# Kernel optimization log

Measured on AMD Instinct MI355X. Metric: run time of the kernel, lower is better.

Reference implementation:

```python
import jax, jax.numpy as jnp
import numpy as np

# Faithful JAX reference for VoxelModule.forward.
# The torch module builds, per batch element, a dict mapping
#   key = vx*10000 + vy*100 + vz  (vx,vy,vz = int(coord * (voxel_size-1)))
# to the list of point indices falling in that voxel.
# Dicts are not jit-able; the equivalent parallel/sort-based grouping is:
#   keys        [B,N] : per-point voxel key (same integer math as torch)
#   order       [B,N] : stable argsort of keys -> point indices grouped by voxel
#   sorted_keys [B,N] : keys in grouped order (run boundaries delimit voxels)
# This (keys, order, sorted_keys) triple encodes exactly the same grouping
# information as the list-of-dicts output.

B = 16
N = 500_000
VOXEL_SIZE = 40  # keys require per-axis index < 100, so voxel_size <= 100


def setup_inputs() -> dict:
    key = jax.random.key(0)
    point_cloud = jax.random.uniform(key, (B, N, 3), dtype=jnp.float32)  # coords in [0,1)
    return {"point_cloud": point_cloud, "voxel_size": VOXEL_SIZE}


def reference(point_cloud, voxel_size):
    # int(x) in Python truncates toward zero; coords are non-negative so
    # truncation == floor. astype(int32) truncates, matching torch code.
    idx = (point_cloud * (voxel_size - 1)).astype(jnp.int32)  # [B,N,3]
    keys = idx[..., 0] * 10000 + idx[..., 1] * 100 + idx[..., 2]  # [B,N]
    # Stable sort: within a voxel, point indices stay in ascending order,
    # matching the append order of the torch dict-building loop.
    order = jnp.argsort(keys, axis=-1, stable=True)  # [B,N] grouped point ids
    sorted_keys = jnp.take_along_axis(keys, order, axis=-1)  # [B,N]
    return keys, order, sorted_keys
```

## Files before the change

### kernel.cpp

```cpp
#include <hip/hip_runtime.h>


#define B 16
#define N 500000
#define BN (B * N)
#define NC2 122
#define RELB 512
#define CAP2 4736
#define TPB1 512
#define NW1 (TPB1 / 64)
#define PPB 8192
#define NG 4
#define CPB ((N + PPB - 1) / PPB)
#define NIT4 3

__global__ __launch_bounds__(TPB1) void pass1(const float* __restrict__ pc,
                                              const int* __restrict__ vs,
                                              int* __restrict__ keys,
                                              int* __restrict__ ccnt,
                                              int* __restrict__ staged) {
    int b = blockIdx.x / CPB;
    int chunk = blockIdx.x % CPB;
    int t = threadIdx.x;
    int w = t >> 6;
    int lane = t & 63;
    __shared__ int lh[NW1][NC2];
    __shared__ int lst[NC2];
    __shared__ int gadj[NC2];
    __shared__ int lim[NC2];
    __shared__ int buf[PPB];
    for (int k = lane; k < NC2; k += 64) lh[w][k] = 0;
    float scale = (float)(vs[0] - 1);
    long gb0 = (long)b * N;
    int pe[4 * NG];
#pragma unroll
    for (int g = 0; g < NG; ++g) {
        int i0 = chunk * PPB + g * 2048 + t * 4;
        if (i0 >= N) continue;
        const float4* F = (const float4*)(pc + 3 * (gb0 + i0));
        float4 f0 = F[0], f1 = F[1], f2 = F[2];
        float xs[4] = {f0.x, f0.w, f1.z, f2.y};
        float ys[4] = {f0.y, f1.x, f1.w, f2.z};
        float zs[4] = {f0.z, f1.y, f2.x, f2.w};
        int kk[4];
#pragma unroll
        for (int j = 0; j < 4; ++j) {
            int vx = (int)(xs[j] * scale);
            int vy = (int)(ys[j] * scale);
            int vz = (int)(zs[j] * scale);
            kk[j] = vx * 10000 + vy * 100 + vz;
            int lin = (vx * 40 + vy) * 40 + vz;
            int c2 = lin >> 9;
            int rv = atomicAdd(&lh[w][c2], 1);
            pe[4 * g + j] = ((lin & 511) << 20) | (c2 << 13) | rv;
        }
        int4 kv; kv.x = kk[0]; kv.y = kk[1]; kv.z = kk[2]; kv.w = kk[3];
        *(int4*)(keys + gb0 + i0) = kv;
    }
    __syncthreads();
    if (t < 64) {
        int idx0 = 2 * t, idx1 = 2 * t + 1;
        int run0 = 0, run1 = 0;
        if (idx0 < NC2) {
#pragma unroll
            for (int ww = 0; ww < NW1; ++ww) { int v = lh[ww][idx0]; lh[ww][idx0] = run0; run0 += v; }
#pragma unroll
            for (int ww = 0; ww < NW1; ++ww) { int v = lh[ww][idx1]; lh[ww][idx1] = run1; run1 += v; }
        }
        int s = run0 + run1;
        int x = s;
#pragma unroll
        for (int d = 1; d < 64; d <<= 1) { int y = __shfl_up(x, d, 64); if (t >= d) x += y; }
        int excl = x - s;
        if (idx0 < NC2) {
            int l0 = excl, l1 = excl + run0;
            lst[idx0] = l0; lst[idx1] = l1;
            int g0 = run0 ? atomicAdd(&ccnt[b * NC2 + idx0], run0) : 0;
            int g1 = run1 ? atomicAdd(&ccnt[b * NC2 + idx1], run1) : 0;
            gadj[idx0] = idx0 * CAP2 + g0 - l0;
            gadj[idx1] = idx1 * CAP2 + g1 - l1;
            lim[idx0] = l0 + CAP2 - g0;
            lim[idx1] = l1 + CAP2 - g1;
        }
    }
    __syncthreads();
#pragma unroll
    for (int g = 0; g < NG; ++g) {
        int i0 = chunk * PPB + g * 2048 + t * 4;
        if (i0 >= N) continue;
#pragma unroll
        for (int j = 0; j < 4; ++j) {
            int e = pe[4 * g + j];
            int c2 = (e >> 13) & 127;
            int rv = e & 8191;
            int rel = e >> 20;
            int pos = lst[c2] + lh[w][c2] + rv;
            buf[pos] = (c2 << 22) | (rel << 13) | (g * 2048 + t * 4 + j);
        }
    }
    __syncthreads();
    int nval = N - chunk * PPB; if (nval > PPB) nval = PPB;
    int ibase = chunk * PPB;
    long sbase = (long)b * NC2 * CAP2;
#pragma unroll
    for (int q = 0; q < PPB / TPB1; ++q) {
        int p = t + q * TPB1;
        if (p < nval) {
            int e = buf[p];
            int c = e >> 22;
            int rel = (e >> 13) & 511;
            int local = e & 8191;
            if (p < lim[c]) staged[sbase + gadj[c] + p] = (rel << 19) | (ibase + local);
        }
    }
}

__global__ __launch_bounds__(512) void pass2(const int* __restrict__ ccnt,
                                             const int* __restrict__ staged,
                                             int* __restrict__ order_out,
                                             int* __restrict__ skeys_out) {
    int bc = blockIdx.x;
    int b = bc / NC2;
    int c2 = bc % NC2;
    int t = threadIdx.x;
    __shared__ int h[RELB];
    __shared__ int st[RELB + 1];
    __shared__ int skeyL[RELB];
    __shared__ int srt[CAP2];
    __shared__ int bsh;
    int cnt = ccnt[bc]; if (cnt > CAP2) cnt = CAP2;
    if (cnt == 0) return;

    {
        int z = t;
        h[z] = 0;
        int lin = (c2 << 9) + z;
        int vx = lin / 1600;
        int r = lin - vx * 1600;
        int vy = r / 40;
        int vz = r - vy * 40;
        skeyL[z] = vx * 10000 + vy * 100 + vz;
    }
    if (t < 64) {
        int idx0 = 2 * t, idx1 = 2 * t + 1;
        int v0 = 0, v1 = 0;
        if (idx0 < NC2) {
            v0 = ccnt[b * NC2 + idx0]; if (v0 > CAP2) v0 = CAP2;
            v1 = ccnt[b * NC2 + idx1]; if (v1 > CAP2) v1 = CAP2;
        }
        int s = v0 + v1;
        int x = s;
#pragma unroll
        for (int d = 1; d < 64; d <<= 1) { int y = __shfl_up(x, d, 64); if (t >= d) x += y; }
        int excl = x - s;
        if (idx0 == c2) bsh = excl;
        if (idx1 == c2) bsh = excl + v0;
    }
    __syncthreads();

    long rb = (long)bc * CAP2;
    const int4* reg4 = (const int4*)(staged + rb);
    int n4 = cnt >> 2;
    int4 ev4[NIT4];
#pragma unroll
    for (int q = 0; q < NIT4; ++q) {
        int p4 = t + q * 512;
        if (p4 < n4) {
            int4 e = reg4[p4];
            ev4[q] = e;
            atomicAdd(&h[e.x >> 19], 1);
            atomicAdd(&h[e.y >> 19], 1);
            atomicAdd(&h[e.z >> 19], 1);
            atomicAdd(&h[e.w >> 19], 1);
        }
    }
    int evt = 0; bool tv = false;
    {
        int p = (n4 << 2) + t;
        if (p < cnt) { evt = staged[rb + p]; tv = true; atomicAdd(&h[evt >> 19], 1); }
    }
    __syncthreads();

    if (t < 64) {
        int vals[8]; int s = 0;
#pragma unroll
        for (int j = 0; j < 8; ++j) { int v = h[8 * t + j]; vals[j] = s; s += v; }
        int x = s;
#pragma unroll
        for (int d = 1; d < 64; d <<= 1) { int y = __shfl_up(x, d, 64); if (t >= d) x += y; }
        int excl = x - s;
#pragma unroll
        for (int j = 0; j < 8; ++j) { st[8 * t + j] = excl + vals[j]; h[8 * t + j] = 0; }
        if (t == 63) st[RELB] = x;
    }
    __syncthreads();

#pragma unroll
    for (int q = 0; q < NIT4; ++q) {
        int p4 = t + q * 512;
        if (p4 < n4) {
            int4 e = ev4[q];
            int z0 = e.x >> 19; srt[st[z0] + atomicAdd(&h[z0], 1)] = e.x;
            int z1 = e.y >> 19; srt[st[z1] + atomicAdd(&h[z1], 1)] = e.y;
            int z2 = e.z >> 19; srt[st[z2] + atomicAdd(&h[z2], 1)] = e.z;
            int z3 = e.w >> 19; srt[st[z3] + atomicAdd(&h[z3], 1)] = e.w;
        }
    }
    if (tv) { int z = evt >> 19; srt[st[z] + atomicAdd(&h[z], 1)] = evt; }
    __syncthreads();

    long ob = (long)b * N + bsh;
    for (int p = t; p < cnt; p += 512) {
        int v = srt[p];
        int z = v >> 19;
        int s = st[z], e2 = st[z + 1];
        int rank = 0;
        for (int j = s; j < e2; ++j) rank += (srt[j] < v);
        order_out[ob + s + rank] = v & 0x7FFFF;
        skeys_out[ob + s + rank] = skeyL[z];
    }
}

extern "C" void kernel_launch(void* const* d_in, const int* in_sizes, int n_in,
                              void* d_out, int out_size, void* d_ws, size_t ws_size,
                              hipStream_t stream) {
    const float* pc = (const float*)d_in[0];
    const int* vs = (const int*)d_in[1];
    int* out = (int*)d_out;
    int* keys_out = out;
    int* order_out = out + BN;
    int* skeys_out = out + 2 * BN;

    int* ccnt = (int*)d_ws;
    int* staged = ccnt + B * NC2;

    (void)hipMemsetAsync(ccnt, 0, (size_t)B * NC2 * sizeof(int), stream);
    pass1<<<B * CPB, TPB1, 0, stream>>>(pc, vs, keys_out, ccnt, staged);
    pass2<<<B * NC2, 512, 0, stream>>>(ccnt, staged, order_out, skeys_out);
}
```

Baseline: 214.0 us.

## Fuse both passes into one kernel with per-batch spin barrier

Merges the binning pass and the per-bucket sort pass into a single persistent-style kernel. Blocks of each batch signal completion through an atomic counter and spin until all chunks of that batch finish, then each block sorts up to two coarse buckets, reusing one shared memory region. This removes a kernel launch and the grid-wide gap between passes, and lets batches progress independently. It relies on all blocks of a batch being co-resident, so it risks deadlock or stalls if occupancy is too low, and busy-waiting blocks hold compute units.

```diff
diff --git a/kernel.cpp b/kernel.cpp
--- a/kernel.cpp
+++ b/kernel.cpp
@@ -13,211 +13,226 @@
 #define NG 4
 #define CPB ((N + PPB - 1) / PPB)
 #define NIT4 3
-
-__global__ __launch_bounds__(TPB1) void pass1(const float* __restrict__ pc,
-                                              const int* __restrict__ vs,
-                                              int* __restrict__ keys,
-                                              int* __restrict__ ccnt,
-                                              int* __restrict__ staged) {
-    int b = blockIdx.x / CPB;
-    int chunk = blockIdx.x % CPB;
+#define SMEM_WORDS (NW1 * NC2 + 3 * NC2 + PPB)
+
+__global__ __launch_bounds__(TPB1, 8) void fused(
+    const float* __restrict__ pc, const int* __restrict__ vs,
+    int* __restrict__ keys, int* __restrict__ ccnt, int* __restrict__ done,
+    int* __restrict__ staged, int* __restrict__ order_out,
+    int* __restrict__ skeys_out) {
+    int blk = blockIdx.x;
+    int b = blk / CPB;
+    int chunk = blk % CPB;
     int t = threadIdx.x;
     int w = t >> 6;
     int lane = t & 63;
-    __shared__ int lh[NW1][NC2];
-    __shared__ int lst[NC2];
-    __shared__ int gadj[NC2];
-    __shared__ int lim[NC2];
-    __shared__ int buf[PPB];
-    for (int k = lane; k < NC2; k += 64) lh[w][k] = 0;
-    float scale = (float)(vs[0] - 1);
-    long gb0 = (long)b * N;
-    int pe[4 * NG];
-#pragma unroll
-    for (int g = 0; g < NG; ++g) {
-        int i0 = chunk * PPB + g * 2048 + t * 4;
-        if (i0 >= N) continue;
-        const float4* F = (const float4*)(pc + 3 * (gb0 + i0));
-        float4 f0 = F[0], f1 = F[1], f2 = F[2];
-        float xs[4] = {f0.x, f0.w, f1.z, f2.y};
-        float ys[4] = {f0.y, f1.x, f1.w, f2.z};
-        float zs[4] = {f0.z, f1.y, f2.x, f2.w};
-        int kk[4];
-#pragma unroll
-        for (int j = 0; j < 4; ++j) {
-            int vx = (int)(xs[j] * scale);
-            int vy = (int)(ys[j] * scale);
-            int vz = (int)(zs[j] * scale);
-            kk[j] = vx * 10000 + vy * 100 + vz;
-            int lin = (vx * 40 + vy) * 40 + vz;
-            int c2 = lin >> 9;
-            int rv = atomicAdd(&lh[w][c2], 1);
-            pe[4 * g + j] = ((lin & 511) << 20) | (c2 << 13) | rv;
-        }
-        int4 kv; kv.x = kk[0]; kv.y = kk[1]; kv.z = kk[2]; kv.w = kk[3];
-        *(int4*)(keys + gb0 + i0) = kv;
+    __shared__ int smem[SMEM_WORDS];
+    __shared__ int bsh;
+
+    {
+        int (*lh)[NC2] = (int(*)[NC2])smem;
+        int* lst = smem + NW1 * NC2;
+        int* gadj = lst + NC2;
+        int* lim = gadj + NC2;
+        int* buf = lim + NC2;
+        for (int k = lane; k < NC2; k += 64) lh[w][k] = 0;
+        float scale = (float)(vs[0] - 1);
+        long gb0 = (long)b * N;
+        int pe[4 * NG];
+#pragma unroll
+        for (int g = 0; g < NG; ++g) {
+            int i0 = chunk * PPB + g * 2048 + t * 4;
+            if (i0 >= N) continue;
+            const float4* F = (const float4*)(pc + 3 * (gb0 + i0));
+            float4 f0 = F[0], f1 = F[1], f2 = F[2];
+            float xs[4] = {f0.x, f0.w, f1.z, f2.y};
+            float ys[4] = {f0.y, f1.x, f1.w, f2.z};
+            float zs[4] = {f0.z, f1.y, f2.x, f2.w};
+            int kk[4];
+#pragma unroll
+            for (int j = 0; j < 4; ++j) {
+                int vx = (int)(xs[j] * scale);
+                int vy = (int)(ys[j] * scale);
+                int vz = (int)(zs[j] * scale);
+                kk[j] = vx * 10000 + vy * 100 + vz;
+                int lin = (vx * 40 + vy) * 40 + vz;
+                int c2 = lin >> 9;
+                int rv = atomicAdd(&lh[w][c2], 1);
+                pe[4 * g + j] = ((lin & 511) << 20) | (c2 << 13) | rv;
+            }
+            int4 kv; kv.x = kk[0]; kv.y = kk[1]; kv.z = kk[2]; kv.w = kk[3];
+            *(int4*)(keys + gb0 + i0) = kv;
+        }
+        __syncthreads();
+        if (t < 64) {
+            int idx0 = 2 * t, idx1 = 2 * t + 1;
+            int run0 = 0, run1 = 0;
+            if (idx0 < NC2) {
+#pragma unroll
+                for (int ww = 0; ww < NW1; ++ww) { int v = lh[ww][idx0]; lh[ww][idx0] = run0; run0 += v; }
+#pragma unroll
+                for (int ww = 0; ww < NW1; ++ww) { int v = lh[ww][idx1]; lh[ww][idx1] = run1; run1 += v; }
+            }
+            int s = run0 + run1;
+            int x = s;
+#pragma unroll
+            for (int d = 1; d < 64; d <<= 1) { int y = __shfl_up(x, d, 64); if (t >= d) x += y; }
+            int excl = x - s;
+            if (idx0 < NC2) {
+                int l0 = excl, l1 = excl + run0;
+                lst[idx0] = l0; lst[idx1] = l1;
+                int g0 = run0 ? atomicAdd(&ccnt[b * NC2 + idx0], run0) : 0;
+                int g1 = run1 ? atomicAdd(&ccnt[b * NC2 + idx1], run1) : 0;
+                gadj[idx0] = idx0 * CAP2 + g0 - l0;
+                gadj[idx1] = idx1 * CAP2 + g1 - l1;
+                lim[idx0] = l0 + CAP2 - g0;
+                lim[idx1] = l1 + CAP2 - g1;
+            }
+        }
+        __syncthreads();
+#pragma unroll
+        for (int g = 0; g < NG; ++g) {
+            int i0 = chunk * PPB + g * 2048 + t * 4;
+            if (i0 >= N) continue;
+#pragma unroll
+            for (int j = 0; j < 4; ++j) {
+                int e = pe[4 * g + j];
+                int c2 = (e >> 13) & 127;
+                int rv = e & 8191;
+                int rel = e >> 20;
+                int pos = lst[c2] + lh[w][c2] + rv;
+                buf[pos] = (c2 << 22) | (rel << 13) | (g * 2048 + t * 4 + j);
+            }
+        }
+        __syncthreads();
+        int nval = N - chunk * PPB; if (nval > PPB) nval = PPB;
+        int ibase = chunk * PPB;
+        long sbase = (long)b * NC2 * CAP2;
+#pragma unroll
+        for (int q = 0; q < PPB / TPB1; ++q) {
+            int p = t + q * TPB1;
+            if (p < nval) {
+                int e = buf[p];
+                int c = e >> 22;
+                int rel = (e >> 13) & 511;
+                int local = e & 8191;
+                if (p < lim[c]) staged[sbase + gadj[c] + p] = (rel << 19) | (ibase + local);
+            }
+        }
     }
     __syncthreads();
-    if (t < 64) {
-        int idx0 = 2 * t, idx1 = 2 * t + 1;
-        int run0 = 0, run1 = 0;
-        if (idx0 < NC2) {
-#pragma unroll
-            for (int ww = 0; ww < NW1; ++ww) { int v = lh[ww][idx0]; lh[ww][idx0] = run0; run0 += v; }
-#pragma unroll
-            for (int ww = 0; ww < NW1; ++ww) { int v = lh[ww][idx1]; lh[ww][idx1] = run1; run1 += v; }
-        }
-        int s = run0 + run1;
-        int x = s;
-#pragma unroll
-        for (int d = 1; d < 64; d <<= 1) { int y = __shfl_up(x, d, 64); if (t >= d) x += y; }
-        int excl = x - s;
-        if (idx0 < NC2) {
-            int l0 = excl, l1 = excl + run0;
-            lst[idx0] = l0; lst[idx1] = l1;
-            int g0 = run0 ? atomicAdd(&ccnt[b * NC2 + idx0], run0) : 0;
-            int g1 = run1 ? atomicAdd(&ccnt[b * NC2 + idx1], run1) : 0;
-            gadj[idx0] = idx0 * CAP2 + g0 - l0;
-            gadj[idx1] = idx1 * CAP2 + g1 - l1;
-            lim[idx0] = l0 + CAP2 - g0;
-            lim[idx1] = l1 + CAP2 - g1;
-        }
+    if (t == 0) {
+        __threadfence();
+        __hip_atomic_fetch_add(&done[b], 1, __ATOMIC_RELEASE, __HIP_MEMORY_SCOPE_AGENT);
+        while (__hip_atomic_load(&done[b], __ATOMIC_RELAXED, __HIP_MEMORY_SCOPE_AGENT) < CPB)
+            __builtin_amdgcn_s_sleep(2);
+        __threadfence();
     }
     __syncthreads();
-#pragma unroll
-    for (int g = 0; g < NG; ++g) {
-        int i0 = chunk * PPB + g * 2048 + t * 4;
-        if (i0 >= N) continue;
-#pragma unroll
-        for (int j = 0; j < 4; ++j) {
-            int e = pe[4 * g + j];
-            int c2 = (e >> 13) & 127;
-            int rv = e & 8191;
-            int rel = e >> 20;
-            int pos = lst[c2] + lh[w][c2] + rv;
-            buf[pos] = (c2 << 22) | (rel << 13) | (g * 2048 + t * 4 + j);
-        }
-    }
-    __syncthreads();
-    int nval = N - chunk * PPB; if (nval > PPB) nval = PPB;
-    int ibase = chunk * PPB;
-    long sbase = (long)b * NC2 * CAP2;
-#pragma unroll
-    for (int q = 0; q < PPB / TPB1; ++q) {
-        int p = t + q * TPB1;
-        if (p < nval) {
-            int e = buf[p];
-            int c = e >> 22;
-            int rel = (e >> 13) & 511;
-            int local = e & 8191;
-            if (p < lim[c]) staged[sbase + gadj[c] + p] = (rel << 19) | (ibase + local);
-        }
-    }
-}
-
-__global__ __launch_bounds__(512) void pass2(const int* __restrict__ ccnt,
-                                             const int* __restrict__ staged,
-                                             int* __restrict__ order_out,
-                                             int* __restrict__ skeys_out) {
-    int bc = blockIdx.x;
-    int b = bc / NC2;
-    int c2 = bc % NC2;
-    int t = threadIdx.x;
-    __shared__ int h[RELB];
-    __shared__ int st[RELB + 1];
-    __shared__ int skeyL[RELB];
-    __shared__ int srt[CAP2];
-    __shared__ int bsh;
-    int cnt = ccnt[bc]; if (cnt > CAP2) cnt = CAP2;
-    if (cnt == 0) return;
 
     {
-        int z = t;
-        h[z] = 0;
-        int lin = (c2 << 9) + z;
-        int vx = lin / 1600;
-        int r = lin - vx * 1600;
-        int vy = r / 40;
-        int vz = r - vy * 40;
-        skeyL[z] = vx * 10000 + vy * 100 + vz;
-    }
-    if (t < 64) {
-        int idx0 = 2 * t, idx1 = 2 * t + 1;
-        int v0 = 0, v1 = 0;
-        if (idx0 < NC2) {
-            v0 = ccnt[b * NC2 + idx0]; if (v0 > CAP2) v0 = CAP2;
-            v1 = ccnt[b * NC2 + idx1]; if (v1 > CAP2) v1 = CAP2;
-        }
-        int s = v0 + v1;
-        int x = s;
-#pragma unroll
-        for (int d = 1; d < 64; d <<= 1) { int y = __shfl_up(x, d, 64); if (t >= d) x += y; }
-        int excl = x - s;
-        if (idx0 == c2) bsh = excl;
-        if (idx1 == c2) bsh = excl + v0;
-    }
-    __syncthreads();
-
-    long rb = (long)bc * CAP2;
-    const int4* reg4 = (const int4*)(staged + rb);
-    int n4 = cnt >> 2;
-    int4 ev4[NIT4];
-#pragma unroll
-    for (int q = 0; q < NIT4; ++q) {
-        int p4 = t + q * 512;
-        if (p4 < n4) {
-            int4 e = reg4[p4];
-            ev4[q] = e;
-            atomicAdd(&h[e.x >> 19], 1);
-            atomicAdd(&h[e.y >> 19], 1);
-            atomicAdd(&h[e.z >> 19], 1);
-            atomicAdd(&h[e.w >> 19], 1);
-        }
-    }
-    int evt = 0; bool tv = false;
-    {
-        int p = (n4 << 2) + t;
-        if (p < cnt) { evt = staged[rb + p]; tv = true; atomicAdd(&h[evt >> 19], 1); }
-    }
-    __syncthreads();
-
-    if (t < 64) {
-        int vals[8]; int s = 0;
-#pragma unroll
-        for (int j = 0; j < 8; ++j) { int v = h[8 * t + j]; vals[j] = s; s += v; }
-        int x = s;
-#pragma unroll
-        for (int d = 1; d < 64; d <<= 1) { int y = __shfl_up(x, d, 64); if (t >= d) x += y; }
-        int excl = x - s;
-#pragma unroll
-        for (int j = 0; j < 8; ++j) { st[8 * t + j] = excl + vals[j]; h[8 * t + j] = 0; }
-        if (t == 63) st[RELB] = x;
-    }
-    __syncthreads();
-
-#pragma unroll
-    for (int q = 0; q < NIT4; ++q) {
-        int p4 = t + q * 512;
-        if (p4 < n4) {
-            int4 e = ev4[q];
-            int z0 = e.x >> 19; srt[st[z0] + atomicAdd(&h[z0], 1)] = e.x;
-            int z1 = e.y >> 19; srt[st[z1] + atomicAdd(&h[z1], 1)] = e.y;
-            int z2 = e.z >> 19; srt[st[z2] + atomicAdd(&h[z2], 1)] = e.z;
-            int z3 = e.w >> 19; srt[st[z3] + atomicAdd(&h[z3], 1)] = e.w;
-        }
-    }
-    if (tv) { int z = evt >> 19; srt[st[z] + atomicAdd(&h[z], 1)] = evt; }
-    __syncthreads();
-
-    long ob = (long)b * N + bsh;
-    for (int p = t; p < cnt; p += 512) {
-        int v = srt[p];
-        int z = v >> 19;
-        int s = st[z], e2 = st[z + 1];
-        int rank = 0;
-        for (int j = s; j < e2; ++j) rank += (srt[j] < v);
-        order_out[ob + s + rank] = v & 0x7FFFF;
-        skeys_out[ob + s + rank] = skeyL[z];
+        int* h = smem;
+        int* st = smem + RELB;
+        int* skeyL = st + RELB + 1;
+        int* srt = skeyL + RELB;
+#pragma unroll 1
+        for (int it = 0; it < 2; ++it) {
+            int c2 = chunk + it * CPB;
+            if (c2 >= NC2) break;
+            int bc = b * NC2 + c2;
+            int cnt = ccnt[bc]; if (cnt > CAP2) cnt = CAP2;
+            __syncthreads();
+            if (cnt == 0) continue;
+
+            {
+                int z = t;
+                h[z] = 0;
+                int lin = (c2 << 9) + z;
+                int vx = lin / 1600;
+                int r = lin - vx * 1600;
+                int vy = r / 40;
+                int vz = r - vy * 40;
+                skeyL[z] = vx * 10000 + vy * 100 + vz;
+            }
+            if (t < 64) {
+                int idx0 = 2 * t, idx1 = 2 * t + 1;
+                int v0 = 0, v1 = 0;
+                if (idx0 < NC2) {
+                    v0 = ccnt[b * NC2 + idx0]; if (v0 > CAP2) v0 = CAP2;
+                    v1 = ccnt[b * NC2 + idx1]; if (v1 > CAP2) v1 = CAP2;
+                }
+                int s = v0 + v1;
+                int x = s;
+#pragma unroll
+                for (int d = 1; d < 64; d <<= 1) { int y = __shfl_up(x, d, 64); if (t >= d) x += y; }
+                int excl = x - s;
+                if (idx0 == c2) bsh = excl;
+                if (idx1 == c2) bsh = excl + v0;
+            }
+            __syncthreads();
+
+            long rb = (long)bc * CAP2;
+            const int4* reg4 = (const int4*)(staged + rb);
+            int n4 = cnt >> 2;
+            int4 ev4[NIT4];
+#pragma unroll
+            for (int q = 0; q < NIT4; ++q) {
+                int p4 = t + q * TPB1;
+                if (p4 < n4) {
+                    int4 e = reg4[p4];
+                    ev4[q] = e;
+                    atomicAdd(&h[e.x >> 19], 1);
+                    atomicAdd(&h[e.y >> 19], 1);
+                    atomicAdd(&h[e.z >> 19], 1);
+                    atomicAdd(&h[e.w >> 19], 1);
+                }
+            }
+            int evt = 0; bool tv = false;
+            {
+                int p = (n4 << 2) + t;
+                if (p < cnt) { evt = staged[rb + p]; tv = true; atomicAdd(&h[evt >> 19], 1); }
+            }
+            __syncthreads();
+
+            if (t < 64) {
+                int vals[8]; int s = 0;
+#pragma unroll
+                for (int j = 0; j < 8; ++j) { int v = h[8 * t + j]; vals[j] = s; s += v; }
+                int x = s;
+#pragma unroll
+                for (int d = 1; d < 64; d <<= 1) { int y = __shfl_up(x, d, 64); if (t >= d) x += y; }
+                int excl = x - s;
+#pragma unroll
+                for (int j = 0; j < 8; ++j) { st[8 * t + j] = excl + vals[j]; h[8 * t + j] = 0; }
+                if (t == 63) st[RELB] = x;
+            }
+            __syncthreads();
+
+#pragma unroll
+            for (int q = 0; q < NIT4; ++q) {
+                int p4 = t + q * TPB1;
+                if (p4 < n4) {
+                    int4 e = ev4[q];
+                    int z0 = e.x >> 19; srt[st[z0] + atomicAdd(&h[z0], 1)] = e.x;
+                    int z1 = e.y >> 19; srt[st[z1] + atomicAdd(&h[z1], 1)] = e.y;
+                    int z2 = e.z >> 19; srt[st[z2] + atomicAdd(&h[z2], 1)] = e.z;
+                    int z3 = e.w >> 19; srt[st[z3] + atomicAdd(&h[z3], 1)] = e.w;
+                }
+            }
+            if (tv) { int z = evt >> 19; srt[st[z] + atomicAdd(&h[z], 1)] = evt; }
+            __syncthreads();
+
+            long ob = (long)b * N + bsh;
+            for (int p = t; p < cnt; p += TPB1) {
+                int v = srt[p];
+                int z = v >> 19;
+                int s = st[z], e2 = st[z + 1];
+                int rank = 0;
+                for (int j = s; j < e2; ++j) rank += (srt[j] < v);
+                order_out[ob + s + rank] = v & 0x7FFFF;
+                skeys_out[ob + s + rank] = skeyL[z];
+            }
+        }
     }
 }
 
@@ -232,9 +247,10 @@
     int* skeys_out = out + 2 * BN;
 
     int* ccnt = (int*)d_ws;
-    int* staged = ccnt + B * NC2;
-
-    (void)hipMemsetAsync(ccnt, 0, (size_t)B * NC2 * sizeof(int), stream);
-    pass1<<<B * CPB, TPB1, 0, stream>>>(pc, vs, keys_out, ccnt, staged);
-    pass2<<<B * NC2, 512, 0, stream>>>(ccnt, staged, order_out, skeys_out);
+    int* done = ccnt + B * NC2;
+    int* staged = done + B;
+
+    (void)hipMemsetAsync(ccnt, 0, (size_t)(B * NC2 + B) * sizeof(int), stream);
+    fused<<<B * CPB, TPB1, 0, stream>>>(pc, vs, keys_out, ccnt, done, staged,
+                                        order_out, skeys_out);
 }
```

New measurement: 382.8 us. 1.79x slower.

## Replace global atomic bucket staging with per-chunk tables and contiguous chunk dumps

Applied to the files above, without the earlier changes.

Pass1 no longer claims global bucket slots with atomics. Each block writes its locally bucket-sorted chunk to staging as contiguous int4 stores and records a per-chunk table of bucket start offsets. Pass2 reads every chunk's offsets for its bucket, prefix-sums them, and gathers elements with a binary search over chunks. This drops the memset, the global atomics and the scattered staging writes. In exchange pass2 does scalar gathers with a per-element binary search, and the chunk index is now packed into fewer bits.

```diff
diff --git a/kernel.cpp b/kernel.cpp
--- a/kernel.cpp
+++ b/kernel.cpp
@@ -7,27 +7,26 @@
 #define NC2 122
 #define RELB 512
 #define CAP2 4736
-#define TPB1 512
-#define NW1 (TPB1 / 64)
+#define TPB 512
+#define NW1 (TPB / 64)
 #define PPB 8192
 #define NG 4
-#define CPB ((N + PPB - 1) / PPB)
-#define NIT4 3
-
-__global__ __launch_bounds__(TPB1) void pass1(const float* __restrict__ pc,
-                                              const int* __restrict__ vs,
-                                              int* __restrict__ keys,
-                                              int* __restrict__ ccnt,
-                                              int* __restrict__ staged) {
+#define CPB 62
+#define LSTROW 128
+#define NIT2 10
+
+__global__ __launch_bounds__(TPB, 8) void pass1(const float* __restrict__ pc,
+                                                const int* __restrict__ vs,
+                                                int* __restrict__ keys,
+                                                int* __restrict__ lstT,
+                                                int* __restrict__ staged) {
     int b = blockIdx.x / CPB;
     int chunk = blockIdx.x % CPB;
     int t = threadIdx.x;
     int w = t >> 6;
     int lane = t & 63;
     __shared__ int lh[NW1][NC2];
-    __shared__ int lst[NC2];
-    __shared__ int gadj[NC2];
-    __shared__ int lim[NC2];
+    __shared__ int lst[NC2 + 1];
     __shared__ int buf[PPB];
     for (int k = lane; k < NC2; k += 64) lh[w][k] = 0;
     float scale = (float)(vs[0] - 1);
@@ -52,7 +51,7 @@
             int lin = (vx * 40 + vy) * 40 + vz;
             int c2 = lin >> 9;
             int rv = atomicAdd(&lh[w][c2], 1);
-            pe[4 * g + j] = ((lin & 511) << 20) | (c2 << 13) | rv;
+            pe[4 * g + j] = (c2 << 22) | ((lin & 511) << 13) | rv;
         }
         int4 kv; kv.x = kk[0]; kv.y = kk[1]; kv.z = kk[2]; kv.w = kk[3];
         *(int4*)(keys + gb0 + i0) = kv;
@@ -72,16 +71,8 @@
 #pragma unroll
         for (int d = 1; d < 64; d <<= 1) { int y = __shfl_up(x, d, 64); if (t >= d) x += y; }
         int excl = x - s;
-        if (idx0 < NC2) {
-            int l0 = excl, l1 = excl + run0;
-            lst[idx0] = l0; lst[idx1] = l1;
-            int g0 = run0 ? atomicAdd(&ccnt[b * NC2 + idx0], run0) : 0;
-            int g1 = run1 ? atomicAdd(&ccnt[b * NC2 + idx1], run1) : 0;
-            gadj[idx0] = idx0 * CAP2 + g0 - l0;
-            gadj[idx1] = idx1 * CAP2 + g1 - l1;
-            lim[idx0] = l0 + CAP2 - g0;
-            lim[idx1] = l1 + CAP2 - g1;
-        }
+        if (idx0 < NC2) { lst[idx0] = excl; lst[idx1] = excl + run0; }
+        if (t == 63) lst[NC2] = x;
     }
     __syncthreads();
 #pragma unroll
@@ -91,31 +82,23 @@
 #pragma unroll
         for (int j = 0; j < 4; ++j) {
             int e = pe[4 * g + j];
-            int c2 = (e >> 13) & 127;
+            int c2 = e >> 22;
             int rv = e & 8191;
-            int rel = e >> 20;
+            int rel = (e >> 13) & 511;
             int pos = lst[c2] + lh[w][c2] + rv;
-            buf[pos] = (c2 << 22) | (rel << 13) | (g * 2048 + t * 4 + j);
-        }
-    }
-    __syncthreads();
-    int nval = N - chunk * PPB; if (nval > PPB) nval = PPB;
-    int ibase = chunk * PPB;
-    long sbase = (long)b * NC2 * CAP2;
-#pragma unroll
-    for (int q = 0; q < PPB / TPB1; ++q) {
-        int p = t + q * TPB1;
-        if (p < nval) {
-            int e = buf[p];
-            int c = e >> 22;
-            int rel = (e >> 13) & 511;
-            int local = e & 8191;
-            if (p < lim[c]) staged[sbase + gadj[c] + p] = (rel << 19) | (ibase + local);
-        }
-    }
+            buf[pos] = (rel << 13) | (g * 2048 + t * 4 + j);
+        }
+    }
+    if (t < NC2 + 1) lstT[(b * CPB + chunk) * LSTROW + t] = lst[t];
+    __syncthreads();
+    long sb4 = (long)(b * CPB + chunk) * (PPB / 4);
+    const int4* B4 = (const int4*)buf;
+    int4* S4 = (int4*)staged;
+#pragma unroll
+    for (int q = 0; q < PPB / TPB / 4; ++q) S4[sb4 + t + q * TPB] = B4[t + q * TPB];
 }
 
-__global__ __launch_bounds__(512) void pass2(const int* __restrict__ ccnt,
+__global__ __launch_bounds__(TPB) void pass2(const int* __restrict__ lstT,
                                              const int* __restrict__ staged,
                                              int* __restrict__ order_out,
                                              int* __restrict__ skeys_out) {
@@ -127,9 +110,9 @@
     __shared__ int st[RELB + 1];
     __shared__ int skeyL[RELB];
     __shared__ int srt[CAP2];
-    __shared__ int bsh;
-    int cnt = ccnt[bc]; if (cnt > CAP2) cnt = CAP2;
-    if (cnt == 0) return;
+    __shared__ int ofs[CPB + 1];
+    __shared__ int adj[CPB];
+    __shared__ int bshS, cntS;
 
     {
         int z = t;
@@ -142,53 +125,52 @@
         skeyL[z] = vx * 10000 + vy * 100 + vz;
     }
     if (t < 64) {
-        int idx0 = 2 * t, idx1 = 2 * t + 1;
-        int v0 = 0, v1 = 0;
-        if (idx0 < NC2) {
-            v0 = ccnt[b * NC2 + idx0]; if (v0 > CAP2) v0 = CAP2;
-            v1 = ccnt[b * NC2 + idx1]; if (v1 > CAP2) v1 = CAP2;
-        }
-        int s = v0 + v1;
+        int s0 = 0, s1 = 0;
+        if (t < CPB) {
+            const int* row = lstT + (b * CPB + t) * LSTROW;
+            s0 = row[c2]; s1 = row[c2 + 1];
+        }
+        int rl = s1 - s0;
+        int bs = s0;
+#pragma unroll
+        for (int d = 1; d < 64; d <<= 1) bs += __shfl_xor(bs, d, 64);
+        int x = rl;
+#pragma unroll
+        for (int d = 1; d < 64; d <<= 1) { int y = __shfl_up(x, d, 64); if (t >= d) x += y; }
+        int excl = x - rl;
+        if (t < CPB) { ofs[t] = excl; adj[t] = t * PPB + s0 - excl; }
+        if (t == CPB - 1) { ofs[CPB] = x; cntS = x; }
+        if (t == 0) bshS = bs;
+    }
+    __syncthreads();
+    int cnt = cntS; if (cnt > CAP2) cnt = CAP2;
+    if (cnt == 0) return;
+    int bsh = bshS;
+    long bbase = (long)b * (CPB * PPB);
+
+    int ev[NIT2];
+#pragma unroll
+    for (int q = 0; q < NIT2; ++q) {
+        int p = t + q * TPB;
+        if (p < cnt) {
+            int lo = 0, hi = CPB;
+            while (hi - lo > 1) { int mid = (lo + hi) >> 1; if (ofs[mid] <= p) lo = mid; else hi = mid; }
+            int e = staged[bbase + adj[lo] + p];
+            int v = ((e >> 13) << 19) | (lo << 13) | (e & 8191);
+            ev[q] = v;
+            atomicAdd(&h[v >> 19], 1);
+        }
+    }
+    __syncthreads();
+
+    if (t < 64) {
+        int vals[8]; int s = 0;
+#pragma unroll
+        for (int j = 0; j < 8; ++j) { int v = h[8 * t + j]; vals[j] = s; s += v; }
         int x = s;
 #pragma unroll
         for (int d = 1; d < 64; d <<= 1) { int y = __shfl_up(x, d, 64); if (t >= d) x += y; }
         int excl = x - s;
-        if (idx0 == c2) bsh = excl;
-        if (idx1 == c2) bsh = excl + v0;
-    }
-    __syncthreads();
-
-    long rb = (long)bc * CAP2;
-    const int4* reg4 = (const int4*)(staged + rb);
-    int n4 = cnt >> 2;
-    int4 ev4[NIT4];
-#pragma unroll
-    for (int q = 0; q < NIT4; ++q) {
-        int p4 = t + q * 512;
-        if (p4 < n4) {
-            int4 e = reg4[p4];
-            ev4[q] = e;
-            atomicAdd(&h[e.x >> 19], 1);
-            atomicAdd(&h[e.y >> 19], 1);
-            atomicAdd(&h[e.z >> 19], 1);
-            atomicAdd(&h[e.w >> 19], 1);
-        }
-    }
-    int evt = 0; bool tv = false;
-    {
-        int p = (n4 << 2) + t;
-        if (p < cnt) { evt = staged[rb + p]; tv = true; atomicAdd(&h[evt >> 19], 1); }
-    }
-    __syncthreads();
-
-    if (t < 64) {
-        int vals[8]; int s = 0;
-#pragma unroll
-        for (int j = 0; j < 8; ++j) { int v = h[8 * t + j]; vals[j] = s; s += v; }
-        int x = s;
-#pragma unroll
-        for (int d = 1; d < 64; d <<= 1) { int y = __shfl_up(x, d, 64); if (t >= d) x += y; }
-        int excl = x - s;
 #pragma unroll
         for (int j = 0; j < 8; ++j) { st[8 * t + j] = excl + vals[j]; h[8 * t + j] = 0; }
         if (t == 63) st[RELB] = x;
@@ -196,21 +178,19 @@
     __syncthreads();
 
 #pragma unroll
-    for (int q = 0; q < NIT4; ++q) {
-        int p4 = t + q * 512;
-        if (p4 < n4) {
-            int4 e = ev4[q];
-            int z0 = e.x >> 19; srt[st[z0] + atomicAdd(&h[z0], 1)] = e.x;
-            int z1 = e.y >> 19; srt[st[z1] + atomicAdd(&h[z1], 1)] = e.y;
-            int z2 = e.z >> 19; srt[st[z2] + atomicAdd(&h[z2], 1)] = e.z;
-            int z3 = e.w >> 19; srt[st[z3] + atomicAdd(&h[z3], 1)] = e.w;
-        }
-    }
-    if (tv) { int z = evt >> 19; srt[st[z] + atomicAdd(&h[z], 1)] = evt; }
+    for (int q = 0; q < NIT2; ++q) {
+        int p = t + q * TPB;
+        if (p < cnt) {
+            int v = ev[q];
+            int z = v >> 19;
+            int r = atomicAdd(&h[z], 1);
+            srt[st[z] + r] = v;
+        }
+    }
     __syncthreads();
 
     long ob = (long)b * N + bsh;
-    for (int p = t; p < cnt; p += 512) {
+    for (int p = t; p < cnt; p += TPB) {
         int v = srt[p];
         int z = v >> 19;
         int s = st[z], e2 = st[z + 1];
@@ -231,10 +211,9 @@
     int* order_out = out + BN;
     int* skeys_out = out + 2 * BN;
 
-    int* ccnt = (int*)d_ws;
-    int* staged = ccnt + B * NC2;
-
-    (void)hipMemsetAsync(ccnt, 0, (size_t)B * NC2 * sizeof(int), stream);
-    pass1<<<B * CPB, TPB1, 0, stream>>>(pc, vs, keys_out, ccnt, staged);
-    pass2<<<B * NC2, 512, 0, stream>>>(ccnt, staged, order_out, skeys_out);
+    int* lstT = (int*)d_ws;
+    int* staged = lstT + B * CPB * LSTROW;
+
+    pass1<<<B * CPB, TPB, 0, stream>>>(pc, vs, keys_out, lstT, staged);
+    pass2<<<B * NC2, TPB, 0, stream>>>(lstT, staged, order_out, skeys_out);
 }
```

Result: no change. 214.4 us (+0.2%).
